# Kernel tuning notes

Measured on AMD Instinct MI355X. Metric: run time of the kernel, lower is better.

The kernel has to match this reference:

```python
import jax, jax.numpy as jnp
import numpy as np

B, T, I, H, HID, NT = 1024, 200, 64, 512, 256, 1


def setup_inputs() -> dict:
    key = jax.random.key(0)
    ks = jax.random.split(key, 12)
    s_h = 1.0 / np.sqrt(H)
    s_i = 1.0 / np.sqrt(I)
    s_hid = 1.0 / np.sqrt(HID)
    return {
        "x": jax.random.normal(ks[0], (B, T, I), dtype=jnp.float32),
        "timestamps": jax.random.uniform(ks[1], (B, T), dtype=jnp.float32),
        # TimeLSTM params: W_all: Linear(H -> 4H), U_all: Linear(I -> 4H), W_d: Linear(H -> H)
        "W_all": jax.random.uniform(ks[2], (4 * H, H), minval=-s_h, maxval=s_h, dtype=jnp.float32),
        "b_all": jax.random.uniform(ks[3], (4 * H,), minval=-s_h, maxval=s_h, dtype=jnp.float32),
        "U_all": jax.random.uniform(ks[4], (4 * H, I), minval=-s_i, maxval=s_i, dtype=jnp.float32),
        "b_u": jax.random.uniform(ks[5], (4 * H,), minval=-s_i, maxval=s_i, dtype=jnp.float32),
        "W_d": jax.random.uniform(ks[6], (H, H), minval=-s_h, maxval=s_h, dtype=jnp.float32),
        "b_d": jax.random.uniform(ks[7], (H,), minval=-s_h, maxval=s_h, dtype=jnp.float32),
        # MLP head: Linear(H -> HID), ReLU, Linear(HID -> NT); dropout in eval mode (identity)
        "W1": jax.random.uniform(ks[8], (HID, H), minval=-s_h, maxval=s_h, dtype=jnp.float32),
        "b1": jax.random.uniform(ks[9], (HID,), minval=-s_h, maxval=s_h, dtype=jnp.float32),
        "W2": jax.random.uniform(ks[10], (NT, HID), minval=-s_hid, maxval=s_hid, dtype=jnp.float32),
        "b2": jax.random.uniform(ks[11], (NT,), minval=-s_hid, maxval=s_hid, dtype=jnp.float32),
    }


def _time_lstm_last_h(x, timestamps, W_all, b_all, U_all, b_u, W_d, b_d):
    # x: [B, T, I], timestamps: [B, T]. Returns final hidden state h_T: [B, H].
    # Precompute input projections for all steps: [T, B, 4H]
    xg = jnp.einsum('bti,gi->tbg', x, U_all) + b_u
    ts = timestamps.T  # [T, B]

    def step(carry, inp):
        h, c = carry
        xgt, tt = inp  # [B, 4H], [B]
        c_s1 = jnp.tanh(c @ W_d.T + b_d)                 # short-term memory
        c_adj = c - c_s1 + c_s1 * tt[:, None]            # time-discounted cell
        gates = h @ W_all.T + b_all + xgt                # [B, 4H]
        f, i, o, c_tmp = jnp.split(jax.nn.sigmoid(gates), 4, axis=1)
        c_new = f * c_adj + i * c_tmp
        h_new = o * jnp.tanh(c_new)
        return (h_new, c_new), None

    h0 = jnp.zeros((x.shape[0], W_d.shape[0]), dtype=x.dtype)
    (h_last, _), _ = jax.lax.scan(step, (h0, h0), (xg, ts))
    return h_last


def reference(x, timestamps, W_all, b_all, U_all, b_u, W_d, b_d, W1, b1, W2, b2):
    h = _time_lstm_last_h(x, timestamps, W_all, b_all, U_all, b_u, W_d, b_d)
    # MLP head (dropout = identity in eval): Linear -> ReLU -> Linear; classification=False so no sigmoid
    hidden = jax.nn.relu(h @ W1.T + b1)
    return hidden @ W2.T + b2  # [B, NT]
```

## Files before the change

kernel.cpp:

```cpp
#include <hip/hip_runtime.h>
#include <cstdint>
#include <cstddef>

#define B_   1024
#define T_   200
#define I_   64
#define H_   512
#define HID_ 256
#define LDA_ 1088
#define NFRAG 88

typedef __bf16 bf16;
typedef __bf16 bf16x4 __attribute__((ext_vector_type(4)));
typedef __bf16 bf16x8 __attribute__((ext_vector_type(8)));
typedef float  f32x4  __attribute__((ext_vector_type(4)));

__device__ inline void gload_lds16(const bf16* g, void* l) {
  void* gg = (void*)g;
  __builtin_amdgcn_global_load_lds((__attribute__((address_space(1))) void*)gg,
                                   (__attribute__((address_space(3))) void*)l,
                                   16, 0, 0);
}

__device__ inline float sigm(float x) { return 1.f / (1.f + __expf(-x)); }
__device__ inline float tanh_f(float x) {
  float e = __expf(2.f * fabsf(x));
  float r = 1.f - 2.f / (e + 1.f);
  return copysignf(r, x);
}
__device__ inline uint32_t bf16bits(float v) {
  union { bf16 h; unsigned short u; } cv; cv.h = (bf16)v; return (uint32_t)cv.u;
}

__global__ __launch_bounds__(512, 2)
void persist(bf16* __restrict__ ping0, bf16* __restrict__ ping1,
             const float* __restrict__ x, const float* __restrict__ tsT,
             const bf16* __restrict__ img,
             const float* __restrict__ ba, const float* __restrict__ bu,
             const float* __restrict__ bd, int* __restrict__ flags)
{
  __shared__ __align__(16) bf16 Wl[NFRAG * 512];

  const int tid = threadIdx.x;
  const int l   = tid & 63, w = tid >> 6;
  const int bid = blockIdx.x;
  const int mt  = bid & 7, jt = bid >> 3;
  const int m0  = mt * 128;
  const int col = l & 15, kh = l >> 4;

  {
    const bf16* src = img + (size_t)jt * (NFRAG * 512);
#pragma unroll
    for (int it = 0; it < 11; ++it)
      gload_lds16(src + it * 4096 + tid * 8, (char*)Wl + it * 8192 + tid * 16);
  }

  float bg[4], bdv;
#pragma unroll
  for (int g = 0; g < 4; ++g) {
    int n = g * 512 + jt * 16 + col;
    bg[g] = ba[n] + bu[n];
  }
  bdv = bd[jt * 16 + col];
  __syncthreads();

  float cst[4] = {0.f, 0.f, 0.f, 0.f};
  const bf16x8* Wf = (const bf16x8*)Wl;

  for (int t = 0; t < T_; ++t) {
    const bf16* Ac = (t & 1) ? ping1 : ping0;
    bf16*       An = (t & 1) ? ping0 : ping1;

    const int rb = m0 + w * 16 + kh * 4;
    float4 tt4 = *(const float4*)(tsT + (size_t)t * B_ + rb);
    const bool dox = (tid < 64) && (t + 1 < T_);
    const int xr = m0 + jt * 4 + (tid >> 4), xc = (tid & 15) * 4;
    float4 xv = {0.f, 0.f, 0.f, 0.f};
    if (dox) xv = *(const float4*)(x + ((size_t)xr * T_ + (t + 1)) * I_ + xc);

    if (t > 0) {
      if (w == 0) {
        int* fl = flags + mt * 32 + (l & 31);
        while (__hip_atomic_load(fl, __ATOMIC_RELAXED,
                                 __HIP_MEMORY_SCOPE_AGENT) < t)
          __builtin_amdgcn_s_sleep(1);
        __builtin_amdgcn_fence(__ATOMIC_ACQUIRE, "agent");
      }
      __syncthreads();
    }

    f32x4 acc[4], accd0, accd1;
#pragma unroll
    for (int g = 0; g < 4; ++g) acc[g] = (f32x4){bg[g], bg[g], bg[g], bg[g]};
    accd0 = (f32x4){bdv, bdv, bdv, bdv};
    accd1 = (f32x4){0.f, 0.f, 0.f, 0.f};

    const size_t ra = (size_t)(m0 + w * 16 + col) * LDA_ + kh * 8;

#pragma unroll
    for (int kk = 0; kk < 18; ++kk) {
      bf16x8 a = *(const bf16x8*)(Ac + ra + kk * 32);
#pragma unroll
      for (int g = 0; g < 4; ++g) {
        bf16x8 bv = Wf[(g * 18 + kk) * 64 + l];
        acc[g] = __builtin_amdgcn_mfma_f32_16x16x32_bf16(a, bv, acc[g], 0, 0, 0);
      }
    }
#pragma unroll
    for (int kk = 0; kk < 16; kk += 2) {
      bf16x8 a0 = *(const bf16x8*)(Ac + ra + 576 + kk * 32);
      bf16x8 a1 = *(const bf16x8*)(Ac + ra + 576 + (kk + 1) * 32);
      accd0 = __builtin_amdgcn_mfma_f32_16x16x32_bf16(a0, Wf[(72 + kk) * 64 + l], accd0, 0, 0, 0);
      accd1 = __builtin_amdgcn_mfma_f32_16x16x32_bf16(a1, Wf[(73 + kk) * 64 + l], accd1, 0, 0, 0);
    }

#pragma unroll
    for (int q = 0; q < 4; ++q) {
      int row   = rb + q;
      float tt  = (&tt4.x)[q];
      float cs1 = tanh_f(accd0[q] + accd1[q]);
      float cadj = cst[q] - cs1 + cs1 * tt;
      float fg = sigm(acc[0][q]);
      float ig = sigm(acc[1][q]);
      float og = sigm(acc[2][q]);
      float cg_ = sigm(acc[3][q]);
      float cn = fg * cadj + ig * cg_;
      float hn = og * tanh_f(cn);
      cst[q] = cn;

      uint32_t hb = bf16bits(hn), cb = bf16bits(cn);
      uint32_t hb2 = (uint32_t)__shfl_xor((int)hb, 1, 64);
      uint32_t cb2 = (uint32_t)__shfl_xor((int)cb, 1, 64);
      if ((l & 1) == 0) {
        uint32_t hwd = hb | (hb2 << 16);
        uint32_t cwd = cb | (cb2 << 16);
        uint32_t* hp = (uint32_t*)(An + (size_t)row * LDA_ + jt * 16 + col);
        uint32_t* cp = (uint32_t*)(An + (size_t)row * LDA_ + 576 + jt * 16 + col);
        __hip_atomic_store(hp, hwd, __ATOMIC_RELAXED, __HIP_MEMORY_SCOPE_AGENT);
        __hip_atomic_store(cp, cwd, __ATOMIC_RELAXED, __HIP_MEMORY_SCOPE_AGENT);
      }
    }

    if (dox) {
      union { bf16 h[4]; unsigned long long u; } pk;
      pk.h[0] = (bf16)xv.x; pk.h[1] = (bf16)xv.y;
      pk.h[2] = (bf16)xv.z; pk.h[3] = (bf16)xv.w;
      unsigned long long* xp =
          (unsigned long long*)(An + (size_t)xr * LDA_ + 512 + xc);
      __hip_atomic_store(xp, pk.u, __ATOMIC_RELAXED, __HIP_MEMORY_SCOPE_AGENT);
    }

    if (t + 1 < T_) {
      __syncthreads();
      if (tid == 0)
        __hip_atomic_store(flags + mt * 32 + jt, t + 1, __ATOMIC_RELAXED,
                           __HIP_MEMORY_SCOPE_AGENT);
    }
  }
}

__global__ void pack_wimg(const float* __restrict__ Wa, const float* __restrict__ Ua,
                          const float* __restrict__ Wd, bf16* __restrict__ img)
{
  int tid = blockIdx.x * 256 + threadIdx.x;
  if (tid >= 32 * NFRAG * 64) return;
  int l  = tid & 63;
  int f  = (tid >> 6) % NFRAG;
  int jt = tid / (NFRAG * 64);
  int col = l & 15, kh = l >> 4;
  float v[8];
  if (f < 72) {
    int g = f / 18, kk = f % 18;
    int n = g * 512 + jt * 16 + col;
    if (kk < 16) {
      int k = kk * 32 + kh * 8;
#pragma unroll
      for (int r = 0; r < 8; ++r) v[r] = Wa[(size_t)n * 512 + k + r];
    } else {
      int k = (kk - 16) * 32 + kh * 8;
#pragma unroll
      for (int r = 0; r < 8; ++r) v[r] = Ua[(size_t)n * 64 + k + r];
    }
  } else {
    int kk = f - 72;
    int n = jt * 16 + col;
    int k = kk * 32 + kh * 8;
#pragma unroll
    for (int r = 0; r < 8; ++r) v[r] = Wd[(size_t)n * 512 + k + r];
  }
  bf16* dst = img + (size_t)tid * 8;
#pragma unroll
  for (int r = 0; r < 8; ++r) dst[r] = (bf16)v[r];
}

__global__ void pack_w1(const float* __restrict__ W1, bf16* __restrict__ W1b)
{
  int idx = blockIdx.x * 256 + threadIdx.x;
  if (idx < HID_ * H_) W1b[idx] = (bf16)W1[idx];
}

__global__ void init_state(const float* __restrict__ x, const float* __restrict__ ts,
                           bf16* __restrict__ Acat, float* __restrict__ tsT,
                           int* __restrict__ flags)
{
  int idx = blockIdx.x * 256 + threadIdx.x;
  if (idx < 8 * 32) flags[idx] = 0;
  if (idx < B_ * T_) {
    int b = idx / T_, t = idx - b * T_;
    tsT[(size_t)t * B_ + b] = ts[idx];
  }
  if (idx >= B_ * LDA_) return;
  int b = idx / LDA_, k = idx - b * LDA_;
  bf16 v = (bf16)0.f;
  if (k >= 512 && k < 576)
    v = (bf16)x[(size_t)b * T_ * I_ + (k - 512)];
  Acat[idx] = v;
}

__global__ __launch_bounds__(256)
void gemm_bf16(const bf16* __restrict__ A, int lda,
               const bf16* __restrict__ W, int ldw,
               float* __restrict__ C, int ldc,
               const float* __restrict__ bias,
               int nsplit, int kb0, int ke0, int kb1, int ke1)
{
  __shared__ __align__(16) bf16 As[128 * 64];
  __shared__ __align__(16) bf16 Bs[128 * 64];

  const int tid  = threadIdx.x;
  const int lane = tid & 63;
  const int wave = tid >> 6;
  const int m0 = blockIdx.y * 128;
  const int n0 = blockIdx.x * 128;
  const int kb = (n0 < nsplit) ? kb0 : kb1;
  const int ke = (n0 < nsplit) ? ke0 : ke1;

  int aoff[4], boff[4];
#pragma unroll
  for (int r = 0; r < 4; ++r) {
    int o16 = r * 256 + tid;
    int row = o16 >> 3;
    int sp  = o16 & 7;
    int s   = sp ^ (row & 7);
    aoff[r] = row * lda + s * 8;
    boff[r] = row * ldw + s * 8;
  }

  f32x4 acc[4][4];
#pragma unroll
  for (int i = 0; i < 4; ++i)
#pragma unroll
    for (int j = 0; j < 4; ++j) acc[i][j] = (f32x4){0.f, 0.f, 0.f, 0.f};

  const int wm = wave >> 1, wn = wave & 1;
  const int r15 = lane & 15, khalf = lane >> 4, sw = lane & 7;

  for (int kt = kb; kt < ke; kt += 64) {
    const bf16* Ag = A + (size_t)m0 * lda + kt;
    const bf16* Wg = W + (size_t)n0 * ldw + kt;
#pragma unroll
    for (int r = 0; r < 4; ++r) {
      char* la = (char*)As + (size_t)(r * 256 + wave * 64) * 16;
      char* lb = (char*)Bs + (size_t)(r * 256 + wave * 64) * 16;
      gload_lds16(Ag + aoff[r], la);
      gload_lds16(Wg + boff[r], lb);
    }
    __syncthreads();

    const bf16x8* Ald = (const bf16x8*)As;
    const bf16x8* Bld = (const bf16x8*)Bs;
#pragma unroll
    for (int kk = 0; kk < 2; ++kk) {
      bf16x8 av[4], bv[4];
#pragma unroll
      for (int i = 0; i < 4; ++i) {
        int ra = wm * 64 + i * 16 + r15;
        av[i] = Ald[ra * 8 + ((kk * 4 + khalf) ^ sw)];
        int rbw = wn * 64 + i * 16 + r15;
        bv[i] = Bld[rbw * 8 + ((kk * 4 + khalf) ^ sw)];
      }
#pragma unroll
      for (int i = 0; i < 4; ++i)
#pragma unroll
        for (int j = 0; j < 4; ++j)
          acc[i][j] = __builtin_amdgcn_mfma_f32_16x16x32_bf16(av[i], bv[j], acc[i][j], 0, 0, 0);
    }
    __syncthreads();
  }

#pragma unroll
  for (int j = 0; j < 4; ++j) {
    int colc = n0 + wn * 64 + j * 16 + r15;
    float bb = bias[colc];
#pragma unroll
    for (int i = 0; i < 4; ++i) {
      int rbase = m0 + wm * 64 + i * 16 + khalf * 4;
#pragma unroll
      for (int q = 0; q < 4; ++q)
        C[(size_t)(rbase + q) * ldc + colc] = acc[i][j][q] + bb;
    }
  }
}

__global__ void mlp_out(const float* __restrict__ Gm, const float* __restrict__ W2,
                        const float* __restrict__ b2, float* __restrict__ out)
{
  int b = blockIdx.x, l = threadIdx.x;
  float s = 0.f;
#pragma unroll
  for (int k = l; k < HID_; k += 64)
    s += fmaxf(Gm[(size_t)b * HID_ + k], 0.f) * W2[k];
#pragma unroll
  for (int off = 32; off; off >>= 1) s += __shfl_xor(s, off, 64);
  if (l == 0) out[b] = s + b2[0];
}

extern "C" void kernel_launch(void* const* d_in, const int* in_sizes, int n_in,
                              void* d_out, int out_size, void* d_ws, size_t ws_size,
                              hipStream_t stream)
{
  const float* x  = (const float*)d_in[0];
  const float* ts = (const float*)d_in[1];
  const float* Wa = (const float*)d_in[2];
  const float* ba = (const float*)d_in[3];
  const float* Ua = (const float*)d_in[4];
  const float* bu = (const float*)d_in[5];
  const float* Wd = (const float*)d_in[6];
  const float* bd = (const float*)d_in[7];
  const float* W1 = (const float*)d_in[8];
  const float* b1 = (const float*)d_in[9];
  const float* W2 = (const float*)d_in[10];
  const float* b2 = (const float*)d_in[11];

  char* ws = (char*)d_ws;
  size_t o = 0;
  auto alloc = [&](size_t bytes) {
    size_t p = o;
    o += (bytes + 255) & ~(size_t)255;
    return p;
  };
  bf16*  Wimg  = (bf16*) (ws + alloc((size_t)32 * NFRAG * 512 * 2));
  bf16*  W1b   = (bf16*) (ws + alloc((size_t)HID_ * H_ * 2));
  bf16*  ping0 = (bf16*) (ws + alloc((size_t)B_ * LDA_ * 2));
  bf16*  ping1 = (bf16*) (ws + alloc((size_t)B_ * LDA_ * 2));
  float* G     = (float*)(ws + alloc((size_t)B_ * HID_ * 4));
  float* tsT   = (float*)(ws + alloc((size_t)B_ * T_ * 4));
  int*   flags = (int*)  (ws + alloc((size_t)8 * 32 * 4));

  pack_wimg<<<(32 * NFRAG * 64 + 255) / 256, 256, 0, stream>>>(Wa, Ua, Wd, Wimg);
  pack_w1<<<(HID_ * H_ + 255) / 256, 256, 0, stream>>>(W1, W1b);
  init_state<<<(B_ * LDA_ + 255) / 256, 256, 0, stream>>>(x, ts, ping0, tsT, flags);

  void* args[] = {(void*)&ping0, (void*)&ping1, (void*)&x, (void*)&tsT,
                  (void*)&Wimg, (void*)&ba, (void*)&bu, (void*)&bd, (void*)&flags};
  hipLaunchCooperativeKernel((void*)persist, dim3(256), dim3(512), args, 0, stream);

  gemm_bf16<<<dim3(HID_ / 128, B_ / 128), 256, 0, stream>>>(
      ping0, LDA_, W1b, H_, G, HID_, b1, 1 << 30, 0, 512, 0, 512);
  mlp_out<<<B_, 64, 0, stream>>>(G, W2, b2, (float*)d_out);
}
```

Baseline: 2.354 ms.

## Split each block into two independent 64-row wave clusters with finer-grained flags

Each persistent block's 8 waves are split into two clusters of 4 waves, each owning 64 batch rows and synchronising through its own set of global flags (16 groups instead of 8). The block-wide __syncthreads before and after each timestep is replaced by per-wave flag spinning and an LDS atomic counter, so the last wave of a cluster publishes the step flag. This aims to reduce barrier stalls and let the two halves of a block progress independently. The cost is more polling traffic, and correctness depends on the vmcnt wait ordering the global stores before the counter increment.

```diff
diff --git a/kernel.cpp b/kernel.cpp
--- a/kernel.cpp
+++ b/kernel.cpp
@@ -9,6 +9,7 @@
 #define HID_ 256
 #define LDA_ 1088
 #define NFRAG 88
+#define NGRP 16
 
 typedef __bf16 bf16;
 typedef __bf16 bf16x4 __attribute__((ext_vector_type(4)));
@@ -40,12 +41,16 @@
              const float* __restrict__ bd, int* __restrict__ flags)
 {
   __shared__ __align__(16) bf16 Wl[NFRAG * 512];
+  __shared__ int scnt[2];
 
   const int tid = threadIdx.x;
   const int l   = tid & 63, w = tid >> 6;
+  const int cl  = w >> 2, wi = w & 3;
   const int bid = blockIdx.x;
-  const int mt  = bid & 7, jt = bid >> 3;
-  const int m0  = mt * 128;
+  const int mt8 = bid & 7, jt = bid >> 3;
+  const int g   = mt8 * 2 + cl;
+  const int m0g = g * 64;
+  const int m0  = m0g + wi * 16;
   const int col = l & 15, kh = l >> 4;
 
   {
@@ -54,12 +59,13 @@
     for (int it = 0; it < 11; ++it)
       gload_lds16(src + it * 4096 + tid * 8, (char*)Wl + it * 8192 + tid * 16);
   }
+  if (tid < 2) scnt[tid] = 0;
 
   float bg[4], bdv;
 #pragma unroll
-  for (int g = 0; g < 4; ++g) {
-    int n = g * 512 + jt * 16 + col;
-    bg[g] = ba[n] + bu[n];
+  for (int gg = 0; gg < 4; ++gg) {
+    int n = gg * 512 + jt * 16 + col;
+    bg[gg] = ba[n] + bu[n];
   }
   bdv = bd[jt * 16 + col];
   __syncthreads();
@@ -71,39 +77,36 @@
     const bf16* Ac = (t & 1) ? ping1 : ping0;
     bf16*       An = (t & 1) ? ping0 : ping1;
 
-    const int rb = m0 + w * 16 + kh * 4;
+    const int rb = m0 + kh * 4;
     float4 tt4 = *(const float4*)(tsT + (size_t)t * B_ + rb);
-    const bool dox = (tid < 64) && (t + 1 < T_);
-    const int xr = m0 + jt * 4 + (tid >> 4), xc = (tid & 15) * 4;
+    const bool dox = (wi == 0) && (l < 32) && (t + 1 < T_);
+    const int xr = m0g + jt * 2 + (l >> 4), xc = (l & 15) * 4;
     float4 xv = {0.f, 0.f, 0.f, 0.f};
     if (dox) xv = *(const float4*)(x + ((size_t)xr * T_ + (t + 1)) * I_ + xc);
 
     if (t > 0) {
-      if (w == 0) {
-        int* fl = flags + mt * 32 + (l & 31);
-        while (__hip_atomic_load(fl, __ATOMIC_RELAXED,
-                                 __HIP_MEMORY_SCOPE_AGENT) < t)
-          __builtin_amdgcn_s_sleep(1);
-        __builtin_amdgcn_fence(__ATOMIC_ACQUIRE, "agent");
-      }
-      __syncthreads();
+      int* fl = flags + g * 32 + (l & 31);
+      while (__hip_atomic_load(fl, __ATOMIC_RELAXED,
+                               __HIP_MEMORY_SCOPE_AGENT) < t)
+        __builtin_amdgcn_s_sleep(1);
+      __builtin_amdgcn_fence(__ATOMIC_ACQUIRE, "agent");
     }
 
     f32x4 acc[4], accd0, accd1;
 #pragma unroll
-    for (int g = 0; g < 4; ++g) acc[g] = (f32x4){bg[g], bg[g], bg[g], bg[g]};
+    for (int gg = 0; gg < 4; ++gg) acc[gg] = (f32x4){bg[gg], bg[gg], bg[gg], bg[gg]};
     accd0 = (f32x4){bdv, bdv, bdv, bdv};
     accd1 = (f32x4){0.f, 0.f, 0.f, 0.f};
 
-    const size_t ra = (size_t)(m0 + w * 16 + col) * LDA_ + kh * 8;
+    const size_t ra = (size_t)(m0 + col) * LDA_ + kh * 8;
 
 #pragma unroll
     for (int kk = 0; kk < 18; ++kk) {
       bf16x8 a = *(const bf16x8*)(Ac + ra + kk * 32);
 #pragma unroll
-      for (int g = 0; g < 4; ++g) {
-        bf16x8 bv = Wf[(g * 18 + kk) * 64 + l];
-        acc[g] = __builtin_amdgcn_mfma_f32_16x16x32_bf16(a, bv, acc[g], 0, 0, 0);
+      for (int gg = 0; gg < 4; ++gg) {
+        bf16x8 bv = Wf[(gg * 18 + kk) * 64 + l];
+        acc[gg] = __builtin_amdgcn_mfma_f32_16x16x32_bf16(a, bv, acc[gg], 0, 0, 0);
       }
     }
 #pragma unroll
@@ -140,7 +143,6 @@
         __hip_atomic_store(cp, cwd, __ATOMIC_RELAXED, __HIP_MEMORY_SCOPE_AGENT);
       }
     }
-
     if (dox) {
       union { bf16 h[4]; unsigned long long u; } pk;
       pk.h[0] = (bf16)xv.x; pk.h[1] = (bf16)xv.y;
@@ -151,10 +153,13 @@
     }
 
     if (t + 1 < T_) {
-      __syncthreads();
-      if (tid == 0)
-        __hip_atomic_store(flags + mt * 32 + jt, t + 1, __ATOMIC_RELAXED,
-                           __HIP_MEMORY_SCOPE_AGENT);
+      asm volatile("s_waitcnt vmcnt(0)" ::: "memory");
+      if (l == 0) {
+        int prev = atomicAdd(&scnt[cl], 1);
+        if (prev == 4 * (t + 1) - 1)
+          __hip_atomic_store(flags + g * 32 + jt, t + 1, __ATOMIC_RELAXED,
+                             __HIP_MEMORY_SCOPE_AGENT);
+      }
     }
   }
 }
@@ -204,7 +209,7 @@
                            int* __restrict__ flags)
 {
   int idx = blockIdx.x * 256 + threadIdx.x;
-  if (idx < 8 * 32) flags[idx] = 0;
+  if (idx < NGRP * 32) flags[idx] = 0;
   if (idx < B_ * T_) {
     int b = idx / T_, t = idx - b * T_;
     tsT[(size_t)t * B_ + b] = ts[idx];
@@ -345,7 +350,7 @@
   bf16*  ping1 = (bf16*) (ws + alloc((size_t)B_ * LDA_ * 2));
   float* G     = (float*)(ws + alloc((size_t)B_ * HID_ * 4));
   float* tsT   = (float*)(ws + alloc((size_t)B_ * T_ * 4));
-  int*   flags = (int*)  (ws + alloc((size_t)8 * 32 * 4));
+  int*   flags = (int*)  (ws + alloc((size_t)NGRP * 32 * 4));
 
   pack_wimg<<<(32 * NFRAG * 64 + 255) / 256, 256, 0, stream>>>(Wa, Ua, Wd, Wimg);
   pack_w1<<<(HID_ * H_ + 255) / 256, 256, 0, stream>>>(W1, W1b);
```

Result: slower. 5.979 ms (+154.0%).
